# Optimization experiments

Hardware: AMD Instinct MI355X
Metric: run time of the kernel (lower is better)

## Reference

```python
import jax, jax.numpy as jnp
import numpy as np

B, C_IN, C_OUT, H, W = 4, 256, 256, 64, 64


def conv1x1(x, w, b):
    # x: [B, Cin, H, W], w: [Cout, Cin], b: [Cout]
    return jnp.einsum('bchw,oc->bohw', x, w) + b[None, :, None, None]


def setup_inputs() -> dict:
    key = jax.random.key(0)
    ks = jax.random.split(key, 12)
    s_in = 1.0 / np.sqrt(C_IN)
    s_out = 1.0 / np.sqrt(C_OUT)
    return {
        'query_input': jax.random.normal(ks[0], (B, C_IN, H, W), jnp.float32),
        'key_value_input': jax.random.normal(ks[1], (B, C_IN, H, W), jnp.float32),
        'Wq': jax.random.uniform(ks[2], (C_OUT, C_IN), jnp.float32, -s_in, s_in),
        'bq': jax.random.uniform(ks[3], (C_OUT,), jnp.float32, -s_in, s_in),
        'Wk': jax.random.uniform(ks[4], (C_OUT, C_IN), jnp.float32, -s_in, s_in),
        'bk': jax.random.uniform(ks[5], (C_OUT,), jnp.float32, -s_in, s_in),
        'Wv': jax.random.uniform(ks[6], (C_OUT, C_IN), jnp.float32, -s_in, s_in),
        'bv': jax.random.uniform(ks[7], (C_OUT,), jnp.float32, -s_in, s_in),
        'W1': jax.random.uniform(ks[8], (C_OUT, C_OUT), jnp.float32, -s_out, s_out),
        'b1': jax.random.uniform(ks[9], (C_OUT,), jnp.float32, -s_out, s_out),
        'W2': jax.random.uniform(ks[10], (C_OUT, C_OUT), jnp.float32, -s_out, s_out),
        'b2': jax.random.uniform(ks[11], (C_OUT,), jnp.float32, -s_out, s_out),
    }


def reference(query_input, key_value_input, Wq, bq, Wk, bk, Wv, bv, W1, b1, W2, b2):
    q = conv1x1(query_input, Wq, bq)            # [B, Co, H, W]
    k = conv1x1(key_value_input, Wk, bk)
    v = conv1x1(key_value_input, Wv, bv)
    b, co, h, w = q.shape
    n = h * w
    qf = q.reshape(b, co, n)                    # [B, Co, N]
    kf = k.reshape(b, co, n)
    vf = v.reshape(b, co, n)
    # scores: q^T k over channels -> [B, N, N], softmax over keys (last dim)
    attn = jax.nn.softmax(jnp.einsum('bcn,bcm->bnm', qf, kf), axis=-1)
    # attended value: [B, Co, N] -> [B, Co, H, W]
    av = jnp.einsum('bnm,bcm->bcn', attn, vf).reshape(b, co, h, w)
    hid = jax.nn.relu(conv1x1(av, W1, b1))
    return conv1x1(hid, W2, b2)
```

## Files before the change

kernel.cpp:

```cpp
#include <hip/hip_runtime.h>
#include <math.h>

#define CCH 256
#define NPIX 4096
#define NB 4
#define NTOT (NB * NPIX)

typedef _Float16 f16;
typedef f16 f16x8 __attribute__((ext_vector_type(8)));
typedef __fp16 fp16x2 __attribute__((ext_vector_type(2)));
typedef float f32x4 __attribute__((ext_vector_type(4)));
typedef unsigned short u16;
typedef unsigned int u32;

__device__ __forceinline__ u16 f2h(float f) {
  union { f16 h; u16 u; } c; c.h = (f16)f; return c.u;
}
__device__ __forceinline__ void fsplit(float v, u16& h, u16& l) {
  union { f16 h; u16 u; } a, b;
  a.h = (f16)v;
  b.h = (f16)(v - (float)a.h);
  h = a.u; l = b.u;
}
__device__ __forceinline__ u32 pkh(float a, float b) {
  union { fp16x2 v; u32 u; } c;
  c.v = __builtin_amdgcn_cvt_pkrtz(a, b);
  return c.u;
}
__device__ __forceinline__ u32 shflu(u32 v, int s) { return (u32)__shfl((int)v, s, 64); }
__device__ __forceinline__ f32x4 mm(f16x8 a, f16x8 b, f32x4 c) {
  return __builtin_amdgcn_mfma_f32_16x16x32_f16(a, b, c, 0, 0, 0);
}
__device__ __forceinline__ f16x8 ld8(const u16* p) {
  return *reinterpret_cast<const f16x8*>(p);
}

using gas_t = const __attribute__((address_space(1))) void*;
using las_t = __attribute__((address_space(3))) void*;
__device__ __forceinline__ void gl2lds16(const void* g, void* l) {
  __builtin_amdgcn_global_load_lds((gas_t)g, (las_t)l, 16, 0, 0);
}

__global__ __launch_bounds__(256) void prep_w(
    const float* w0, const float* w1, const float* w2, const float* w3,
    const float* w4, u16* wp)
{
  const float* srcs[5] = {w0, w1, w2, w3, w4};
  const int m = blockIdx.y;
  const float* s = srcs[m];
  u16* ph = wp + (size_t)m * 2 * 65536;
  u16* pl = ph + 65536;
  const int i = (blockIdx.x * 256 + threadIdx.x) * 4;
  float4 v = *reinterpret_cast<const float4*>(s + i);
  ushort4 hv, lv;
  fsplit(v.x, hv.x, lv.x); fsplit(v.y, hv.y, lv.y);
  fsplit(v.z, hv.z, lv.z); fsplit(v.w, hv.w, lv.w);
  *reinterpret_cast<ushort4*>(ph + i) = hv;
  *reinterpret_cast<ushort4*>(pl + i) = lv;
}

__global__ __launch_bounds__(256) void transpose_split(
    const float* xq, const float* xkv,
    u16* xqTh, u16* xqTl, u16* xkvTh, u16* xkvTl)
{
  __shared__ float T[64][65];
  const int nb = blockIdx.x * 64, cb = blockIdx.y * 64;
  const int z = blockIdx.z, b = z & 3, inp = z >> 2;
  const float* src = (inp ? xkv : xq) + (size_t)b * CCH * NPIX;
  u16* dh = inp ? xkvTh : xqTh;
  u16* dl = inp ? xkvTl : xqTl;
  const int t = threadIdx.x;
  #pragma unroll
  for (int k = 0; k < 4; ++k) {
    int e = t + 256 * k;
    int c = e >> 4, n4 = e & 15;
    float4 v = *reinterpret_cast<const float4*>(&src[(size_t)(cb + c) * NPIX + nb + n4 * 4]);
    T[c][n4 * 4 + 0] = v.x; T[c][n4 * 4 + 1] = v.y;
    T[c][n4 * 4 + 2] = v.z; T[c][n4 * 4 + 3] = v.w;
  }
  __syncthreads();
  const int n = t >> 2, cq = t & 3, c0 = cq * 16;
  alignas(16) u16 hh[16], ll[16];
  #pragma unroll
  for (int j = 0; j < 16; ++j) fsplit(T[c0 + j][n], hh[j], ll[j]);
  size_t base = ((size_t)b * NPIX + nb + n) * CCH + cb + c0;
  *reinterpret_cast<uint4*>(&dh[base])     = *reinterpret_cast<uint4*>(hh);
  *reinterpret_cast<uint4*>(&dh[base + 8]) = *reinterpret_cast<uint4*>(hh + 8);
  *reinterpret_cast<uint4*>(&dl[base])     = *reinterpret_cast<uint4*>(ll);
  *reinterpret_cast<uint4*>(&dl[base + 8]) = *reinterpret_cast<uint4*>(ll + 8);
}

template<int PL, int OM>
__global__ __launch_bounds__(512) void conv_s0(
    const u16* __restrict__ Ah, const u16* __restrict__ Al,
    const u16* __restrict__ Wh, const u16* __restrict__ Wl,
    const float* __restrict__ bias, u16* __restrict__ Oh, u16* __restrict__ Ol)
{
  __shared__ alignas(16) u16 sA[PL * 64 * 256];
  const int nb = blockIdx.x * 64, ob = blockIdx.y * 128;
  const int tid = threadIdx.x, wid = tid >> 6, lane = tid & 63;
  const int gg = lane >> 4, x = lane & 15;
  const int wn = wid & 1, wo = wid >> 1;

  f16x8 bh[2][8], bl[2][8];
  #pragma unroll
  for (int os = 0; os < 2; ++os) {
    const int row = ob + wo * 32 + os * 16 + x;
    #pragma unroll
    for (int kc = 0; kc < 8; ++kc) {
      bh[os][kc] = ld8(&Wh[(size_t)row * 256 + kc * 32 + gg * 8]);
      bl[os][kc] = ld8(&Wl[(size_t)row * 256 + kc * 32 + gg * 8]);
    }
  }
  const u16* Ap[2] = {Ah, Al};
  #pragma unroll
  for (int p = 0; p < PL; ++p)
    #pragma unroll
    for (int r = 0; r < 4; ++r) {
      int e = tid + 512 * r;
      int row = e >> 5, ch = e & 31;
      gl2lds16(Ap[p] + (size_t)(nb + row) * 256 + ((ch ^ (row & 7)) * 8),
               &sA[p * 16384 + e * 8]);
    }
  __syncthreads();

  f32x4 acc[2][2] = {};
  #pragma unroll
  for (int ms = 0; ms < 2; ++ms) {
    const int row = wn * 32 + ms * 16 + x;
    #pragma unroll
    for (int kc = 0; kc < 8; ++kc) {
      const int off = row * 256 + ((kc * 4 + gg) ^ (x & 7)) * 8;
      f16x8 a0 = ld8(&sA[off]);
      #pragma unroll
      for (int os = 0; os < 2; ++os) {
        acc[ms][os] = mm(a0, bh[os][kc], acc[ms][os]);
        acc[ms][os] = mm(a0, bl[os][kc], acc[ms][os]);
      }
      if (PL == 2) {
        f16x8 a1 = ld8(&sA[16384 + off]);
        #pragma unroll
        for (int os = 0; os < 2; ++os)
          acc[ms][os] = mm(a1, bh[os][kc], acc[ms][os]);
      }
    }
  }
  #pragma unroll
  for (int os = 0; os < 2; ++os) {
    const float bo = bias[ob + wo * 32 + os * 16 + x];
    const size_t col = ob + wo * 32 + os * 16 + x;
    #pragma unroll
    for (int ms = 0; ms < 2; ++ms)
      #pragma unroll
      for (int j = 0; j < 4; ++j) {
        float val = acc[ms][os][j] + bo;
        size_t row = nb + wn * 32 + ms * 16 + gg * 4 + j;
        if (OM == 1) {
          Oh[row * 256 + col] = f2h(fmaxf(val, 0.f));
        } else {
          u16 h, l; fsplit(val, h, l);
          Oh[row * 256 + col] = h;
          Ol[row * 256 + col] = l;
        }
      }
  }
}

template<int PL, int OM>
__global__ __launch_bounds__(512) void conv_s1(
    const u16* __restrict__ Wh, const u16* __restrict__ Wl,
    const u16* __restrict__ Bh, const u16* __restrict__ Bl,
    const float* __restrict__ bias, void* __restrict__ Out)
{
  __shared__ alignas(16) u16 sB[PL * 64 * 256];
  const int nb = blockIdx.x * 64, ob = blockIdx.y * 128;
  const int tid = threadIdx.x, wid = tid >> 6, lane = tid & 63;
  const int gg = lane >> 4, x = lane & 15;
  const int wn = wid & 1, wo = wid >> 1;

  f16x8 ah[2][8], al[2][8];
  #pragma unroll
  for (int as = 0; as < 2; ++as) {
    const int row = ob + wo * 32 + as * 16 + x;
    #pragma unroll
    for (int kc = 0; kc < 8; ++kc) {
      ah[as][kc] = ld8(&Wh[(size_t)row * 256 + kc * 32 + gg * 8]);
      al[as][kc] = ld8(&Wl[(size_t)row * 256 + kc * 32 + gg * 8]);
    }
  }
  const u16* Bp[2] = {Bh, Bl};
  #pragma unroll
  for (int p = 0; p < PL; ++p)
    #pragma unroll
    for (int r = 0; r < 4; ++r) {
      int e = tid + 512 * r;
      int row = e >> 5, ch = e & 31;
      gl2lds16(Bp[p] + (size_t)(nb + row) * 256 + ((ch ^ (row & 7)) * 8),
               &sB[p * 16384 + e * 8]);
    }
  __syncthreads();

  f32x4 acc[2][2] = {};
  #pragma unroll
  for (int ns = 0; ns < 2; ++ns) {
    const int row = wn * 32 + ns * 16 + x;
    #pragma unroll
    for (int kc = 0; kc < 8; ++kc) {
      const int off = row * 256 + ((kc * 4 + gg) ^ (x & 7)) * 8;
      f16x8 b0 = ld8(&sB[off]);
      #pragma unroll
      for (int as = 0; as < 2; ++as) {
        acc[as][ns] = mm(ah[as][kc], b0, acc[as][ns]);
        acc[as][ns] = mm(al[as][kc], b0, acc[as][ns]);
      }
      if (PL == 2) {
        f16x8 b1 = ld8(&sB[16384 + off]);
        #pragma unroll
        for (int as = 0; as < 2; ++as)
          acc[as][ns] = mm(ah[as][kc], b1, acc[as][ns]);
      }
    }
  }
  #pragma unroll
  for (int as = 0; as < 2; ++as)
    #pragma unroll
    for (int j = 0; j < 4; ++j) {
      const int o = ob + wo * 32 + as * 16 + gg * 4 + j;
      const float bo = bias[o];
      #pragma unroll
      for (int ns = 0; ns < 2; ++ns) {
        int nf = nb + wn * 32 + ns * 16 + x;
        float val = acc[as][ns][j] + bo;
        int b_ = nf >> 12, n_ = nf & 4095;
        size_t addr = ((size_t)b_ * 256 + o) * 4096 + n_;
        if (OM == 1) ((float*)Out)[addr] = val;
        else         ((u16*)Out)[addr] = f2h(val);
      }
    }
}

__global__ __launch_bounds__(512) void attn_mfma(
    const u16* __restrict__ Qh, const u16* __restrict__ Ql,
    const u16* __restrict__ Kh, const u16* __restrict__ Kl,
    const u16* __restrict__ Vs, u16* __restrict__ AVt)
{
  __shared__ alignas(16) u16 smem[49152];
  __shared__ float sMm[2][64], sMl[2][64];
  u16* sKh = smem;
  u16* sKl = smem + 16384;
  u16* sV  = smem + 32768;

  const int b = blockIdx.y, qb = blockIdx.x * 64;
  const int tid = threadIdx.x, wid = tid >> 6;
  const int g = wid & 3, par = wid >> 2;
  const int lane = tid & 63, gg = lane >> 4, x = lane & 15;

  f16x8 qh[8], ql[8];
  {
    const u16* qhp = Qh + ((size_t)b * NPIX + qb + g * 16 + x) * CCH;
    const u16* qlp = Ql + ((size_t)b * NPIX + qb + g * 16 + x) * CCH;
    #pragma unroll
    for (int kc = 0; kc < 8; ++kc) {
      qh[kc] = ld8(qhp + kc * 32 + gg * 8);
      ql[kc] = ld8(qlp + kc * 32 + gg * 8);
    }
  }
  int kSrc[4], kDst[4], vSrc[4], vDst[4];
  #pragma unroll
  for (int r = 0; r < 4; ++r) {
    int e = tid + 512 * r;
    int m = e >> 5, ch = e & 31;
    kSrc[r] = m * CCH + ((ch ^ (m & 7)) * 8);
    kDst[r] = e * 8;
    int c = e >> 3, c2 = e & 7;
    vSrc[r] = c * NPIX + ((c2 ^ (c & 7)) * 8);
    vDst[r] = e * 8;
  }
  const u16* KhB = Kh + (size_t)b * NPIX * CCH;
  const u16* KlB = Kl + (size_t)b * NPIX * CCH;
  const u16* VB  = Vs + (size_t)b * CCH * NPIX;

  f32x4 Oacc[16];
  #pragma unroll
  for (int i = 0; i < 16; ++i) Oacc[i] = f32x4{0.f, 0.f, 0.f, 0.f};
  float m_run = -INFINITY, l_run = 0.f;

  #pragma unroll
  for (int r = 0; r < 4; ++r) {
    gl2lds16(KhB + kSrc[r], &sKh[kDst[r]]);
    gl2lds16(KlB + kSrc[r], &sKl[kDst[r]]);
    gl2lds16(VB + vSrc[r], &sV[vDst[r]]);
  }
  __syncthreads();

  for (int mt = 0; mt < 64; ++mt) {
    f32x4 St[2];
    St[0] = f32x4{0.f, 0.f, 0.f, 0.f};
    St[1] = f32x4{0.f, 0.f, 0.f, 0.f};
    #pragma unroll
    for (int msub = 0; msub < 2; ++msub) {
      const int rb = (par * 32 + msub * 16 + x) * CCH;
      #pragma unroll
      for (int kc = 0; kc < 8; ++kc) {
        const int off = rb + ((kc * 4 + gg) ^ (x & 7)) * 8;
        f16x8 ah_ = ld8(&sKh[off]);
        f16x8 al_ = ld8(&sKl[off]);
        St[msub] = mm(ah_, qh[kc], St[msub]);
        St[msub] = mm(ah_, ql[kc], St[msub]);
        St[msub] = mm(al_, qh[kc], St[msub]);
      }
    }
    __syncthreads();

    if (mt + 1 < 64) {
      const size_t ko = (size_t)(mt + 1) * 64 * CCH;
      #pragma unroll
      for (int r = 0; r < 4; ++r) {
        gl2lds16(KhB + ko + kSrc[r], &sKh[kDst[r]]);
        gl2lds16(KlB + ko + kSrc[r], &sKl[kDst[r]]);
      }
    }

    float vmax = fmaxf(fmaxf(fmaxf(St[0][0], St[0][1]), fmaxf(St[0][2], St[0][3])),
                       fmaxf(fmaxf(St[1][0], St[1][1]), fmaxf(St[1][2], St[1][3])));
    vmax = fmaxf(vmax, __shfl_xor(vmax, 16, 64));
    vmax = fmaxf(vmax, __shfl_xor(vmax, 32, 64));
    float alpha = 1.f;
    if (!__all(vmax <= m_run + 8.f)) {
      const float mnew = fmaxf(m_run, vmax);
      alpha = __expf(m_run - mnew);
      m_run = mnew;
      #pragma unroll
      for (int i = 0; i < 16; ++i) Oacc[i] *= alpha;
    }
    float p[2][4], ps = 0.f;
    #pragma unroll
    for (int msx = 0; msx < 2; ++msx)
      #pragma unroll
      for (int r = 0; r < 4; ++r) {
        p[msx][r] = __expf(St[msx][r] - m_run);
        ps += p[msx][r];
      }
    ps += __shfl_xor(ps, 16, 64);
    ps += __shfl_xor(ps, 32, 64);
    l_run = l_run * alpha + ps;

    u32 Pp[2][2];
    #pragma unroll
    for (int msx = 0; msx < 2; ++msx) {
      Pp[msx][0] = pkh(p[msx][0], p[msx][1]);
      Pp[msx][1] = pkh(p[msx][2], p[msx][3]);
    }
    const int src0 = ((gg & 1) * 2) * 16 + x, src1 = src0 + 16;
    const bool sel = (gg >> 1) != 0;
    union { u32 u[4]; f16x8 v; } pb;
    {
      u32 a0 = shflu(Pp[0][0], src0), a1 = shflu(Pp[1][0], src0);
      u32 b0 = shflu(Pp[0][1], src0), b1 = shflu(Pp[1][1], src0);
      u32 c0 = shflu(Pp[0][0], src1), c1 = shflu(Pp[1][0], src1);
      u32 d0 = shflu(Pp[0][1], src1), d1 = shflu(Pp[1][1], src1);
      pb.u[0] = sel ? a1 : a0;
      pb.u[1] = sel ? b1 : b0;
      pb.u[2] = sel ? c1 : c0;
      pb.u[3] = sel ? d1 : d0;
    }

    #pragma unroll
    for (int cs = 0; cs < 16; ++cs) {
      const int off = (cs * 16 + x) * 64 + ((par * 4 + gg) ^ (x & 7)) * 8;
      Oacc[cs] = mm(ld8(&sV[off]), pb.v, Oacc[cs]);
    }
    __syncthreads();

    if (mt + 1 < 64) {
      const size_t vo = (size_t)(mt + 1) * 64;
      #pragma unroll
      for (int r = 0; r < 4; ++r)
        gl2lds16(VB + vo + vSrc[r], &sV[vDst[r]]);
    }
  }

  const int q = g * 16 + x;
  if (gg == 0) { sMm[par][q] = m_run; sMl[par][q] = l_run; }
  __syncthreads();
  const float mo = sMm[1 - par][q], lo = sMl[1 - par][q];
  const float mtot = fmaxf(m_run, mo);
  const float w = __expf(m_run - mtot), wo_ = __expf(mo - mtot);
  const float lt = l_run * w + lo * wo_;
  const float sc = w / lt;
  #pragma unroll
  for (int i = 0; i < 16; ++i) Oacc[i] *= sc;

  float* Obuf = reinterpret_cast<float*>(smem);
  #define OFF_(G, C, X) ((G) * 4360 + (C) * 17 + (X))
  if (par == 1) {
    #pragma unroll
    for (int cs = 0; cs < 16; ++cs)
      #pragma unroll
      for (int r = 0; r < 4; ++r)
        Obuf[OFF_(g, cs * 16 + gg * 4 + r, x)] = Oacc[cs][r];
  }
  __syncthreads();
  if (par == 0) {
    #pragma unroll
    for (int cs = 0; cs < 16; ++cs)
      #pragma unroll
      for (int r = 0; r < 4; ++r)
        Obuf[OFF_(g, cs * 16 + gg * 4 + r, x)] += Oacc[cs][r];
  }
  __syncthreads();
  const int n_loc = tid & 63, cq = tid >> 6;
  const int g2 = n_loc >> 4, x2 = n_loc & 15, c0 = cq * 32;
  alignas(16) u32 wds[16];
  #pragma unroll
  for (int j = 0; j < 16; ++j)
    wds[j] = pkh(Obuf[OFF_(g2, c0 + 2 * j, x2)], Obuf[OFF_(g2, c0 + 2 * j + 1, x2)]);
  u16* dst = AVt + ((size_t)b * NPIX + qb + n_loc) * CCH + c0;
  #pragma unroll
  for (int k = 0; k < 4; ++k)
    *reinterpret_cast<uint4*>(dst + k * 8) = *reinterpret_cast<uint4*>(&wds[k * 4]);
}

extern "C" void kernel_launch(void* const* d_in, const int* in_sizes, int n_in,
                              void* d_out, int out_size, void* d_ws, size_t ws_size,
                              hipStream_t stream) {
  const float* x_q  = (const float*)d_in[0];
  const float* x_kv = (const float*)d_in[1];
  const float* Wq = (const float*)d_in[2];
  const float* bq = (const float*)d_in[3];
  const float* Wk = (const float*)d_in[4];
  const float* bk = (const float*)d_in[5];
  const float* Wv = (const float*)d_in[6];
  const float* bv = (const float*)d_in[7];
  const float* W1 = (const float*)d_in[8];
  const float* b1 = (const float*)d_in[9];
  const float* W2 = (const float*)d_in[10];
  const float* b2 = (const float*)d_in[11];
  float* out = (float*)d_out;

  u16* ws = (u16*)d_ws;
  const size_t P = (size_t)NTOT * CCH;
  u16* xqTh  = ws;
  u16* xqTl  = ws + P;
  u16* xkvTh = ws + 2 * P;
  u16* xkvTl = ws + 3 * P;
  u16* Wp    = ws + 4 * P;
  u16* Whq = Wp + 0 * 65536, *Wlq = Wp + 1 * 65536;
  u16* Whk = Wp + 2 * 65536, *Wlk = Wp + 3 * 65536;
  u16* Whv = Wp + 4 * 65536, *Wlv = Wp + 5 * 65536;
  u16* Wh1 = Wp + 6 * 65536, *Wl1 = Wp + 7 * 65536;
  u16* Wh2 = Wp + 8 * 65536, *Wl2 = Wp + 9 * 65536;
  u16* base2 = Wp + 10 * 65536;
  u16* Qhp = base2 + 0 * P;
  u16* Qlp = base2 + 1 * P;
  u16* Khp = base2 + 2 * P;
  u16* Klp = base2 + 3 * P;
  u16* Vhp = base2 + 4 * P;
  u16* AVt  = xqTh;
  u16* HIDt = xqTl;

  prep_w<<<dim3(64, 5), 256, 0, stream>>>(Wq, Wk, Wv, W1, W2, Wp);
  transpose_split<<<dim3(64, 4, 8), 256, 0, stream>>>(
      x_q, x_kv, xqTh, xqTl, xkvTh, xkvTl);

  conv_s0<2, 0><<<dim3(256, 2), 512, 0, stream>>>(xqTh, xqTl, Whq, Wlq, bq, Qhp, Qlp);
  conv_s0<2, 0><<<dim3(256, 2), 512, 0, stream>>>(xkvTh, xkvTl, Whk, Wlk, bk, Khp, Klp);
  conv_s1<2, 0><<<dim3(256, 2), 512, 0, stream>>>(Whv, Wlv, xkvTh, xkvTl, bv, (void*)Vhp);

  attn_mfma<<<dim3(NPIX / 64, NB), 512, 0, stream>>>(Qhp, Qlp, Khp, Klp, Vhp, AVt);

  conv_s0<1, 1><<<dim3(256, 2), 512, 0, stream>>>(AVt, nullptr, Wh1, Wl1, b1, HIDt, nullptr);
  conv_s1<1, 1><<<dim3(256, 2), 512, 0, stream>>>(Wh2, Wl2, HIDt, nullptr, b2, (void*)out);
}
```

Baseline: 398.1 us.

## Fold Q projection into K via Wq^T Wk and software-pipeline attention barriers

Rewrites the attention scores algebraically as xq^T (Wq^T Wk) xkv plus a per-key bias term (Wk^T bq · xkv), dropping the constant bk terms that cancel in the softmax. This removes the separate Q projection conv: a small fp32 GEMM builds M = Wq^T Wk, one conv computes Y = M·xkv, and a GEMV produces the per-key bias vector u that the attention kernel adds to each score tile. The attention kernel also swaps __syncthreads for explicit waitcnt and barrier sequences so the next K/V tile loads overlap compute. The changed arithmetic path can alter numerical error, and the hand-placed vmcnt counts must match the number of outstanding loads.

```diff
diff --git a/kernel.cpp b/kernel.cpp
--- a/kernel.cpp
+++ b/kernel.cpp
@@ -41,11 +41,64 @@
   __builtin_amdgcn_global_load_lds((gas_t)g, (las_t)l, 16, 0, 0);
 }
 
+#define SB()  __builtin_amdgcn_sched_barrier(0)
+#define BARN() __builtin_amdgcn_s_barrier()
+#define ASMW(s) asm volatile("s_waitcnt " s ::: "memory")
+
+__global__ __launch_bounds__(256) void mm_wqwk(
+    const float* __restrict__ Wq, const float* __restrict__ Wk,
+    float* __restrict__ M)
+{
+  __shared__ float Aq[32][68], Ak[32][68];
+  const int c1b = blockIdx.x * 64, c2b = blockIdx.y * 64;
+  const int t = threadIdx.x, ty = t >> 4, tx = t & 15;
+  float acc[4][4] = {};
+  for (int os = 0; os < 256; os += 32) {
+    __syncthreads();
+    #pragma unroll
+    for (int k = 0; k < 2; ++k) {
+      int e = t + 256 * k, row = e >> 4, c4 = e & 15;
+      *reinterpret_cast<float4*>(&Aq[row][c4 * 4]) =
+          *reinterpret_cast<const float4*>(&Wq[(size_t)(os + row) * 256 + c1b + c4 * 4]);
+      *reinterpret_cast<float4*>(&Ak[row][c4 * 4]) =
+          *reinterpret_cast<const float4*>(&Wk[(size_t)(os + row) * 256 + c2b + c4 * 4]);
+    }
+    __syncthreads();
+    #pragma unroll
+    for (int o = 0; o < 32; ++o) {
+      float4 a = *reinterpret_cast<const float4*>(&Aq[o][ty * 4]);
+      float4 b = *reinterpret_cast<const float4*>(&Ak[o][tx * 4]);
+      const float av[4] = {a.x, a.y, a.z, a.w};
+      const float bv[4] = {b.x, b.y, b.z, b.w};
+      #pragma unroll
+      for (int i = 0; i < 4; ++i)
+        #pragma unroll
+        for (int j = 0; j < 4; ++j)
+          acc[i][j] = fmaf(av[i], bv[j], acc[i][j]);
+    }
+  }
+  #pragma unroll
+  for (int i = 0; i < 4; ++i) {
+    float4 r; r.x = acc[i][0]; r.y = acc[i][1]; r.z = acc[i][2]; r.w = acc[i][3];
+    *reinterpret_cast<float4*>(&M[(size_t)(c1b + ty * 4 + i) * 256 + c2b + tx * 4]) = r;
+  }
+}
+
+__global__ __launch_bounds__(256) void gvec(
+    const float* __restrict__ Wk, const float* __restrict__ bq,
+    float* __restrict__ g)
+{
+  const int c = threadIdx.x;
+  float s = 0.f;
+  for (int o = 0; o < 256; ++o) s = fmaf(Wk[(size_t)o * 256 + c], bq[o], s);
+  g[c] = s;
+}
+
 __global__ __launch_bounds__(256) void prep_w(
     const float* w0, const float* w1, const float* w2, const float* w3,
-    const float* w4, u16* wp)
-{
-  const float* srcs[5] = {w0, w1, w2, w3, w4};
+    u16* wp)
+{
+  const float* srcs[4] = {w0, w1, w2, w3};
   const int m = blockIdx.y;
   const float* s = srcs[m];
   u16* ph = wp + (size_t)m * 2 * 65536;
@@ -90,6 +143,33 @@
   *reinterpret_cast<uint4*>(&dl[base + 8]) = *reinterpret_cast<uint4*>(ll + 8);
 }
 
+__global__ __launch_bounds__(256) void u_gemv(
+    const u16* __restrict__ xh, const u16* __restrict__ xl,
+    const float* __restrict__ g, float* __restrict__ u)
+{
+  __shared__ float sg[256];
+  sg[threadIdx.x] = g[threadIdx.x];
+  __syncthreads();
+  const int wid = threadIdx.x >> 6, lane = threadIdx.x & 63;
+  const int rl = lane >> 4, x = lane & 15;
+  const int row = blockIdx.x * 16 + wid * 4 + rl;
+  const int c0 = x * 16;
+  const u16* ph = xh + (size_t)row * 256 + c0;
+  const u16* pl = xl + (size_t)row * 256 + c0;
+  f16x8 h0 = ld8(ph), h1 = ld8(ph + 8), l0 = ld8(pl), l1 = ld8(pl + 8);
+  float s = 0.f;
+  #pragma unroll
+  for (int j = 0; j < 8; ++j) {
+    s = fmaf((float)h0[j] + (float)l0[j], sg[c0 + j], s);
+    s = fmaf((float)h1[j] + (float)l1[j], sg[c0 + 8 + j], s);
+  }
+  s += __shfl_xor(s, 1, 64);
+  s += __shfl_xor(s, 2, 64);
+  s += __shfl_xor(s, 4, 64);
+  s += __shfl_xor(s, 8, 64);
+  if (x == 0) u[row] = s;
+}
+
 template<int PL, int OM>
 __global__ __launch_bounds__(512) void conv_s0(
     const u16* __restrict__ Ah, const u16* __restrict__ Al,
@@ -130,7 +210,7 @@
     const int row = wn * 32 + ms * 16 + x;
     #pragma unroll
     for (int kc = 0; kc < 8; ++kc) {
-      const int off = row * 256 + ((kc * 4 + gg) ^ (x & 7)) * 8;
+      const int off = row * 256 + (((kc * 4 + gg) ^ (x & 7)) * 8);
       f16x8 a0 = ld8(&sA[off]);
       #pragma unroll
       for (int os = 0; os < 2; ++os) {
@@ -147,7 +227,7 @@
   }
   #pragma unroll
   for (int os = 0; os < 2; ++os) {
-    const float bo = bias[ob + wo * 32 + os * 16 + x];
+    const float bo = bias ? bias[ob + wo * 32 + os * 16 + x] : 0.f;
     const size_t col = ob + wo * 32 + os * 16 + x;
     #pragma unroll
     for (int ms = 0; ms < 2; ++ms)
@@ -206,7 +286,7 @@
     const int row = wn * 32 + ns * 16 + x;
     #pragma unroll
     for (int kc = 0; kc < 8; ++kc) {
-      const int off = row * 256 + ((kc * 4 + gg) ^ (x & 7)) * 8;
+      const int off = row * 256 + (((kc * 4 + gg) ^ (x & 7)) * 8);
       f16x8 b0 = ld8(&sB[off]);
       #pragma unroll
       for (int as = 0; as < 2; ++as) {
@@ -242,9 +322,12 @@
 __global__ __launch_bounds__(512) void attn_mfma(
     const u16* __restrict__ Qh, const u16* __restrict__ Ql,
     const u16* __restrict__ Kh, const u16* __restrict__ Kl,
-    const u16* __restrict__ Vs, u16* __restrict__ AVt)
+    const u16* __restrict__ Vs,
+    const float* __restrict__ uB,
+    u16* __restrict__ AVt)
 {
   __shared__ alignas(16) u16 smem[49152];
+  __shared__ alignas(16) float sU[4096];
   __shared__ float sMm[2][64], sMl[2][64];
   u16* sKh = smem;
   u16* sKl = smem + 16384;
@@ -279,19 +362,35 @@
   const u16* KhB = Kh + (size_t)b * NPIX * CCH;
   const u16* KlB = Kl + (size_t)b * NPIX * CCH;
   const u16* VB  = Vs + (size_t)b * CCH * NPIX;
+  const char* uBb = (const char*)(uB + (size_t)b * NPIX);
+
+#define STAGE_K(KO) do {                                        \
+    _Pragma("unroll")                                           \
+    for (int r_ = 0; r_ < 4; ++r_) {                            \
+      size_t src_ = (KO) + kSrc[r_];                            \
+      gl2lds16(KhB + src_, &sKh[kDst[r_]]);                     \
+      gl2lds16(KlB + src_, &sKl[kDst[r_]]);                     \
+    } } while (0)
+
+#define STAGE_V(VO) do {                                        \
+    _Pragma("unroll")                                           \
+    for (int r_ = 0; r_ < 4; ++r_)                              \
+      gl2lds16(VB + (VO) + vSrc[r_], &sV[vDst[r_]]);            \
+    } while (0)
 
   f32x4 Oacc[16];
   #pragma unroll
   for (int i = 0; i < 16; ++i) Oacc[i] = f32x4{0.f, 0.f, 0.f, 0.f};
   float m_run = -INFINITY, l_run = 0.f;
 
-  #pragma unroll
-  for (int r = 0; r < 4; ++r) {
-    gl2lds16(KhB + kSrc[r], &sKh[kDst[r]]);
-    gl2lds16(KlB + kSrc[r], &sKl[kDst[r]]);
-    gl2lds16(VB + vSrc[r], &sV[vDst[r]]);
-  }
-  __syncthreads();
+  STAGE_K((size_t)0);
+  STAGE_V((size_t)0);
+  #pragma unroll
+  for (int j = 0; j < 2; ++j) {
+    int e = tid + 512 * j;
+    gl2lds16(uBb + e * 16, &sU[e * 4]);
+  }
+  ASMW("vmcnt(0)"); SB(); BARN(); SB();
 
   for (int mt = 0; mt < 64; ++mt) {
     f32x4 St[2];
@@ -302,7 +401,7 @@
       const int rb = (par * 32 + msub * 16 + x) * CCH;
       #pragma unroll
       for (int kc = 0; kc < 8; ++kc) {
-        const int off = rb + ((kc * 4 + gg) ^ (x & 7)) * 8;
+        const int off = rb + (((kc * 4 + gg) ^ (x & 7)) * 8);
         f16x8 ah_ = ld8(&sKh[off]);
         f16x8 al_ = ld8(&sKl[off]);
         St[msub] = mm(ah_, qh[kc], St[msub]);
@@ -310,16 +409,15 @@
         St[msub] = mm(al_, qh[kc], St[msub]);
       }
     }
-    __syncthreads();
-
-    if (mt + 1 < 64) {
-      const size_t ko = (size_t)(mt + 1) * 64 * CCH;
-      #pragma unroll
-      for (int r = 0; r < 4; ++r) {
-        gl2lds16(KhB + ko + kSrc[r], &sKh[kDst[r]]);
-        gl2lds16(KlB + ko + kSrc[r], &sKl[kDst[r]]);
-      }
-    }
+    {
+      f32x4 u0 = *reinterpret_cast<const f32x4*>(&sU[mt * 64 + par * 32 + gg * 4]);
+      f32x4 u1 = *reinterpret_cast<const f32x4*>(&sU[mt * 64 + par * 32 + 16 + gg * 4]);
+      St[0] += u0;
+      St[1] += u1;
+    }
+    ASMW("lgkmcnt(0)"); SB(); BARN(); SB();
+
+    STAGE_K((size_t)((mt + 1) & 63) * (64 * CCH));
 
     float vmax = fmaxf(fmaxf(fmaxf(St[0][0], St[0][1]), fmaxf(St[0][2], St[0][3])),
                        fmaxf(fmaxf(St[1][0], St[1][1]), fmaxf(St[1][2], St[1][3])));
@@ -365,24 +463,25 @@
       pb.u[3] = sel ? d1 : d0;
     }
 
+    ASMW("vmcnt(8)"); SB(); BARN(); SB();
+
     #pragma unroll
     for (int cs = 0; cs < 16; ++cs) {
-      const int off = (cs * 16 + x) * 64 + ((par * 4 + gg) ^ (x & 7)) * 8;
+      const int off = (cs * 16 + x) * 64 + (((par * 4 + gg) ^ (x & 7)) * 8);
       Oacc[cs] = mm(ld8(&sV[off]), pb.v, Oacc[cs]);
     }
-    __syncthreads();
-
-    if (mt + 1 < 64) {
-      const size_t vo = (size_t)(mt + 1) * 64;
-      #pragma unroll
-      for (int r = 0; r < 4; ++r)
-        gl2lds16(VB + vo + vSrc[r], &sV[vDst[r]]);
-    }
-  }
+    ASMW("lgkmcnt(0)"); SB(); BARN(); SB();
+
+    STAGE_V((size_t)((mt + 1) & 63) * 64);
+
+    ASMW("vmcnt(4)"); SB(); BARN(); SB();
+  }
+
+  ASMW("vmcnt(0) lgkmcnt(0)"); SB(); BARN(); SB();
 
   const int q = g * 16 + x;
   if (gg == 0) { sMm[par][q] = m_run; sMl[par][q] = l_run; }
-  __syncthreads();
+  ASMW("lgkmcnt(0)"); SB(); BARN(); SB();
   const float mo = sMm[1 - par][q], lo = sMl[1 - par][q];
   const float mtot = fmaxf(m_run, mo);
   const float w = __expf(m_run - mtot), wo_ = __expf(mo - mtot);
@@ -400,7 +499,7 @@
       for (int r = 0; r < 4; ++r)
         Obuf[OFF_(g, cs * 16 + gg * 4 + r, x)] = Oacc[cs][r];
   }
-  __syncthreads();
+  ASMW("lgkmcnt(0)"); SB(); BARN(); SB();
   if (par == 0) {
     #pragma unroll
     for (int cs = 0; cs < 16; ++cs)
@@ -408,7 +507,7 @@
       for (int r = 0; r < 4; ++r)
         Obuf[OFF_(g, cs * 16 + gg * 4 + r, x)] += Oacc[cs][r];
   }
-  __syncthreads();
+  ASMW("lgkmcnt(0)"); SB(); BARN(); SB();
   const int n_loc = tid & 63, cq = tid >> 6;
   const int g2 = n_loc >> 4, x2 = n_loc & 15, c0 = cq * 32;
   alignas(16) u32 wds[16];
@@ -437,6 +536,7 @@
   const float* W2 = (const float*)d_in[10];
   const float* b2 = (const float*)d_in[11];
   float* out = (float*)d_out;
+  (void)bk;
 
   u16* ws = (u16*)d_ws;
   const size_t P = (size_t)NTOT * CCH;
@@ -445,30 +545,36 @@
   u16* xkvTh = ws + 2 * P;
   u16* xkvTl = ws + 3 * P;
   u16* Wp    = ws + 4 * P;
-  u16* Whq = Wp + 0 * 65536, *Wlq = Wp + 1 * 65536;
-  u16* Whk = Wp + 2 * 65536, *Wlk = Wp + 3 * 65536;
-  u16* Whv = Wp + 4 * 65536, *Wlv = Wp + 5 * 65536;
-  u16* Wh1 = Wp + 6 * 65536, *Wl1 = Wp + 7 * 65536;
-  u16* Wh2 = Wp + 8 * 65536, *Wl2 = Wp + 9 * 65536;
-  u16* base2 = Wp + 10 * 65536;
-  u16* Qhp = base2 + 0 * P;
-  u16* Qlp = base2 + 1 * P;
-  u16* Khp = base2 + 2 * P;
-  u16* Klp = base2 + 3 * P;
-  u16* Vhp = base2 + 4 * P;
-  u16* AVt  = xqTh;
-  u16* HIDt = xqTl;
-
-  prep_w<<<dim3(64, 5), 256, 0, stream>>>(Wq, Wk, Wv, W1, W2, Wp);
+  u16* Mh  = Wp + 0 * 65536, *Ml  = Wp + 1 * 65536;
+  u16* Wvh = Wp + 2 * 65536, *Wvl = Wp + 3 * 65536;
+  u16* W1h = Wp + 4 * 65536, *W1l = Wp + 5 * 65536;
+  u16* W2h = Wp + 6 * 65536, *W2l = Wp + 7 * 65536;
+  float* Mf32 = (float*)(Wp + 8 * 65536);
+  float* gv   = (float*)(Wp + 8 * 65536 + 131072);
+  float* uB   = (float*)(Wp + 8 * 65536 + 131584);
+  u16* Yh  = ws + 5 * P;
+  u16* Yl  = ws + 6 * P;
+  u16* Vhp = ws + 7 * P;
+  u16* AVt = ws + 8 * P;
+  u16* HIDt = xqTh;
+
+  mm_wqwk<<<dim3(4, 4), 256, 0, stream>>>(Wq, Wk, Mf32);
+  gvec<<<1, 256, 0, stream>>>(Wk, bq, gv);
   transpose_split<<<dim3(64, 4, 8), 256, 0, stream>>>(
       x_q, x_kv, xqTh, xqTl, xkvTh, xkvTl);
-
-  conv_s0<2, 0><<<dim3(256, 2), 512, 0, stream>>>(xqTh, xqTl, Whq, Wlq, bq, Qhp, Qlp);
-  conv_s0<2, 0><<<dim3(256, 2), 512, 0, stream>>>(xkvTh, xkvTl, Whk, Wlk, bk, Khp, Klp);
-  conv_s1<2, 0><<<dim3(256, 2), 512, 0, stream>>>(Whv, Wlv, xkvTh, xkvTl, bv, (void*)Vhp);
-
-  attn_mfma<<<dim3(NPIX / 64, NB), 512, 0, stream>>>(Qhp, Qlp, Khp, Klp, Vhp, AVt);
-
-  conv_s0<1, 1><<<dim3(256, 2), 512, 0, stream>>>(AVt, nullptr, Wh1, Wl1, b1, HIDt, nullptr);
-  conv_s1<1, 1><<<dim3(256, 2), 512, 0, stream>>>(Wh2, Wl2, HIDt, nullptr, b2, (void*)out);
-}
+  prep_w<<<dim3(64, 4), 256, 0, stream>>>(Mf32, Wv, W1, W2, Wp);
+
+  conv_s0<2, 0><<<dim3(256, 2), 512, 0, stream>>>(
+      xkvTh, xkvTl, Mh, Ml, nullptr, Yh, Yl);
+  conv_s1<2, 0><<<dim3(256, 2), 512, 0, stream>>>(
+      Wvh, Wvl, xkvTh, xkvTl, bv, (void*)Vhp);
+  u_gemv<<<dim3(NTOT / 16), 256, 0, stream>>>(xkvTh, xkvTl, gv, uB);
+
+  attn_mfma<<<dim3(NPIX / 64, NB), 512, 0, stream>>>(
+      xqTh, xqTl, Yh, Yl, Vhp, uB, AVt);
+
+  conv_s0<1, 1><<<dim3(256, 2), 512, 0, stream>>>(
+      AVt, nullptr, W1h, W1l, b1, HIDt, nullptr);
+  conv_s1<1, 1><<<dim3(256, 2), 512, 0, stream>>>(
+      W2h, W2l, HIDt, nullptr, b2, (void*)out);
+}
```

Result: slower. 406.7 us (+2.2%).
